# Kernel optimization log

Hardware: AMD Instinct MI355X
Metric: run time of the kernel (lower is better)

## Reference

```python
import jax, jax.numpy as jnp
import numpy as np

B, H, D = 4096, 200, 32


def setup_inputs() -> dict:
    key = jax.random.key(0)
    k1, k2 = jax.random.split(key)
    pred = jax.random.normal(k1, (B, H, D), dtype=jnp.float32)
    targ = jax.random.normal(k2, (B, H, D), dtype=jnp.float32)
    return {"pred": pred, "targ": targ}


def reference(pred, targ):
    # mask out positions where target is exactly zero (padding convention)
    mask = (targ != 0).astype(pred.dtype)
    # per-sample sum of masked squared error, then mean over batch.
    # NOTE: the original module also builds a 'masked' indicator tensor via a
    # per-batch Python loop with .item() syncs, but it never affects the loss
    # (dead code), so it is dropped here. The 'weights' buffer is also unused.
    per_sample = jnp.sum((pred - targ) ** 2 * mask, axis=(1, 2))  # [B]
    weighted_loss = jnp.mean(per_sample)
    return (weighted_loss, weighted_loss)  # (loss, a0_loss) — dict value in original
```

## Files before the change

### kernel.cpp

```cpp
#include <hip/hip_runtime.h>


#define BLOCK 256
#define GRID 2048

__global__ void wsl_init(double* ws) {
    if (blockIdx.x == 0 && threadIdx.x == 0) ws[0] = 0.0;
}

__global__ __launch_bounds__(BLOCK) void wsl_reduce(const float4* __restrict__ pred,
                                                    const float4* __restrict__ targ,
                                                    double* __restrict__ ws,
                                                    long n4) {
    long idx = (long)blockIdx.x * blockDim.x + threadIdx.x;
    long stride = (long)gridDim.x * blockDim.x;
    float acc = 0.0f;
    for (long i = idx; i < n4; i += stride) {
        float4 p = pred[i];
        float4 t = targ[i];
        float d0 = p.x - t.x;
        float d1 = p.y - t.y;
        float d2 = p.z - t.z;
        float d3 = p.w - t.w;
        acc += (t.x != 0.0f) ? d0 * d0 : 0.0f;
        acc += (t.y != 0.0f) ? d1 * d1 : 0.0f;
        acc += (t.z != 0.0f) ? d2 * d2 : 0.0f;
        acc += (t.w != 0.0f) ? d3 * d3 : 0.0f;
    }
    #pragma unroll
    for (int off = 32; off > 0; off >>= 1)
        acc += __shfl_down(acc, off, 64);

    __shared__ float wsum[BLOCK / 64];
    int lane = threadIdx.x & 63;
    int wid  = threadIdx.x >> 6;
    if (lane == 0) wsum[wid] = acc;
    __syncthreads();
    if (threadIdx.x == 0) {
        float s = 0.0f;
        #pragma unroll
        for (int i = 0; i < BLOCK / 64; ++i) s += wsum[i];
        atomicAdd(ws, (double)s);
    }
}

__global__ void wsl_finalize(const double* __restrict__ ws, float* __restrict__ out,
                             double inv_b) {
    if (blockIdx.x == 0 && threadIdx.x == 0) {
        float v = (float)(ws[0] * inv_b);
        out[0] = v;
        out[1] = v;
    }
}

extern "C" void kernel_launch(void* const* d_in, const int* in_sizes, int n_in,
                              void* d_out, int out_size, void* d_ws, size_t ws_size,
                              hipStream_t stream) {
    const float4* pred = (const float4*)d_in[0];
    const float4* targ = (const float4*)d_in[1];
    float* out = (float*)d_out;
    double* ws = (double*)d_ws;

    const long n_elems = (long)in_sizes[0];
    const long n4 = n_elems / 4;
    const double inv_b = 1.0 / 4096.0;

    wsl_init<<<1, 64, 0, stream>>>(ws);
    wsl_reduce<<<GRID, BLOCK, 0, stream>>>(pred, targ, ws, n4);
    wsl_finalize<<<1, 64, 0, stream>>>(ws, out, inv_b);
}
```

Baseline: 230.6 us.

## Replace grid-stride atomic reduction with one-shot blocks and a two-pass partial sum

```diff
diff --git a/kernel.cpp b/kernel.cpp
--- a/kernel.cpp
+++ b/kernel.cpp
@@ -2,31 +2,35 @@
 
 
 #define BLOCK 256
-#define GRID 2048
+#define UNROLL 4
 
-__global__ void wsl_init(double* ws) {
-    if (blockIdx.x == 0 && threadIdx.x == 0) ws[0] = 0.0;
-}
+__global__ __launch_bounds__(BLOCK) void wsl_partials(const float4* __restrict__ pred,
+                                                      const float4* __restrict__ targ,
+                                                      float* __restrict__ partials,
+                                                      long n4) {
+    long base = (long)blockIdx.x * (BLOCK * UNROLL) + threadIdx.x;
 
-__global__ __launch_bounds__(BLOCK) void wsl_reduce(const float4* __restrict__ pred,
-                                                    const float4* __restrict__ targ,
-                                                    double* __restrict__ ws,
-                                                    long n4) {
-    long idx = (long)blockIdx.x * blockDim.x + threadIdx.x;
-    long stride = (long)gridDim.x * blockDim.x;
+    float4 p[UNROLL], t[UNROLL];
+    #pragma unroll
+    for (int k = 0; k < UNROLL; ++k) {
+        long i = base + (long)k * BLOCK;
+        p[k] = pred[i];
+        t[k] = targ[i];
+    }
+
     float acc = 0.0f;
-    for (long i = idx; i < n4; i += stride) {
-        float4 p = pred[i];
-        float4 t = targ[i];
-        float d0 = p.x - t.x;
-        float d1 = p.y - t.y;
-        float d2 = p.z - t.z;
-        float d3 = p.w - t.w;
-        acc += (t.x != 0.0f) ? d0 * d0 : 0.0f;
-        acc += (t.y != 0.0f) ? d1 * d1 : 0.0f;
-        acc += (t.z != 0.0f) ? d2 * d2 : 0.0f;
-        acc += (t.w != 0.0f) ? d3 * d3 : 0.0f;
+    #pragma unroll
+    for (int k = 0; k < UNROLL; ++k) {
+        float d0 = p[k].x - t[k].x;
+        float d1 = p[k].y - t[k].y;
+        float d2 = p[k].z - t[k].z;
+        float d3 = p[k].w - t[k].w;
+        acc += (t[k].x != 0.0f) ? d0 * d0 : 0.0f;
+        acc += (t[k].y != 0.0f) ? d1 * d1 : 0.0f;
+        acc += (t[k].z != 0.0f) ? d2 * d2 : 0.0f;
+        acc += (t[k].w != 0.0f) ? d3 * d3 : 0.0f;
     }
+
     #pragma unroll
     for (int off = 32; off > 0; off >>= 1)
         acc += __shfl_down(acc, off, 64);
@@ -40,14 +44,32 @@
         float s = 0.0f;
         #pragma unroll
         for (int i = 0; i < BLOCK / 64; ++i) s += wsum[i];
-        atomicAdd(ws, (double)s);
+        partials[blockIdx.x] = s;
     }
 }
 
-__global__ void wsl_finalize(const double* __restrict__ ws, float* __restrict__ out,
-                             double inv_b) {
-    if (blockIdx.x == 0 && threadIdx.x == 0) {
-        float v = (float)(ws[0] * inv_b);
+__global__ __launch_bounds__(BLOCK) void wsl_final(const float* __restrict__ partials,
+                                                   int nblocks,
+                                                   float* __restrict__ out,
+                                                   double inv_b) {
+    double acc = 0.0;
+    for (int i = threadIdx.x; i < nblocks; i += BLOCK)
+        acc += (double)partials[i];
+
+    #pragma unroll
+    for (int off = 32; off > 0; off >>= 1)
+        acc += __shfl_down(acc, off, 64);
+
+    __shared__ double wsum[BLOCK / 64];
+    int lane = threadIdx.x & 63;
+    int wid  = threadIdx.x >> 6;
+    if (lane == 0) wsum[wid] = acc;
+    __syncthreads();
+    if (threadIdx.x == 0) {
+        double s = 0.0;
+        #pragma unroll
+        for (int i = 0; i < BLOCK / 64; ++i) s += wsum[i];
+        float v = (float)(s * inv_b);
         out[0] = v;
         out[1] = v;
     }
@@ -59,13 +81,12 @@
     const float4* pred = (const float4*)d_in[0];
     const float4* targ = (const float4*)d_in[1];
     float* out = (float*)d_out;
-    double* ws = (double*)d_ws;
+    float* partials = (float*)d_ws;
 
     const long n_elems = (long)in_sizes[0];
     const long n4 = n_elems / 4;
-    const double inv_b = 1.0 / 4096.0;
+    const int  nblocks = (int)(n4 / (BLOCK * UNROLL));
 
-    wsl_init<<<1, 64, 0, stream>>>(ws);
-    wsl_reduce<<<GRID, BLOCK, 0, stream>>>(pred, targ, ws, n4);
-    wsl_finalize<<<1, 64, 0, stream>>>(ws, out, inv_b);
+    wsl_partials<<<nblocks, BLOCK, 0, stream>>>(pred, targ, partials, n4);
+    wsl_final<<<1, BLOCK, 0, stream>>>(partials, nblocks, out, 1.0 / 4096.0);
 }
```

After: 223.6 us. 3.1% less time.
